# Kernel tuning notes

Hardware: AMD Instinct MI355X
Metric: run time of the kernel (lower is better)

Reference implementation:

```python
import jax, jax.numpy as jnp
import numpy as np

N = 20        # number_of_nodes
K = 2         # Chebyshev order
E_DIM = 4     # embedding_dimensions
OUT = 2       # out_channels
F_IN = 8      # node_features
B = 131072    # batch


def setup_inputs() -> dict:
    key = jax.random.key(0)
    ks = jax.random.split(key, 8)
    x = jax.random.normal(ks[0], (B, N, F_IN), jnp.float32)
    e = jax.random.normal(ks[1], (N, E_DIM), jnp.float32)
    # AVWGCN parameter pools: weights_pool (E_DIM, K, in, out), bias_pool (E_DIM, out)
    gate_w = jax.random.normal(ks[2], (E_DIM, K, F_IN + OUT, 2 * OUT), jnp.float32) * 0.1
    gate_b = jax.random.normal(ks[3], (E_DIM, 2 * OUT), jnp.float32) * 0.1
    upd_w = jax.random.normal(ks[4], (E_DIM, K, F_IN + OUT, OUT), jnp.float32) * 0.1
    upd_b = jax.random.normal(ks[5], (E_DIM, OUT), jnp.float32) * 0.1
    lin_w = jax.random.normal(ks[6], (1, OUT), jnp.float32) * 0.5
    lin_b = jax.random.normal(ks[7], (1,), jnp.float32) * 0.1
    return {"x": x, "e": e, "gate_w": gate_w, "gate_b": gate_b,
            "upd_w": upd_w, "upd_b": upd_b, "lin_w": lin_w, "lin_b": lin_b}


def _avwgcn(x, e, supports, w_pool, b_pool):
    # Node-adaptive weights: (N, K, in, out) and bias (N, out)
    W = jnp.einsum('nd,dkio->nkio', e, w_pool)
    b = e @ b_pool
    # K-hop graph conv gather: (B, N, K, in)
    x_g = jnp.einsum('knm,bmc->bnkc', supports, x)
    return jnp.einsum('bnki,nkio->bno', x_g, W) + b


def reference(x, e, gate_w, gate_b, upd_w, upd_b, lin_w, lin_b):
    dt = x.dtype
    # Adaptive adjacency: softmax(relu(E E^T)) rows; Chebyshev set for K=2 is [I, A]
    A = jax.nn.softmax(jax.nn.relu(e @ e.T), axis=1)
    supports = jnp.stack([jnp.eye(N, dtype=dt), A.astype(dt)])  # (K, N, N)

    H = jnp.zeros((x.shape[0], N, OUT), dt)  # self.h is None -> zeros
    XH = jnp.concatenate([x, H], axis=-1)
    ZR = jax.nn.sigmoid(_avwgcn(XH, e, supports, gate_w, gate_b))
    Z, R = ZR[..., :OUT], ZR[..., OUT:]
    C = jnp.concatenate([x, Z * H], axis=-1)
    HC = jnp.tanh(_avwgcn(C, e, supports, upd_w, upd_b))
    H = R * H + (1.0 - R) * HC

    y = jax.nn.relu(H)
    y = y @ lin_w.T + lin_b
    return y
```

## Files before the change

kernel.cpp:

```cpp
#include <hip/hip_runtime.h>
#include <math.h>

#define NN 20
#define ED 4
#define XROW 160
#define NC 80
#define NKT 5
#define NNT 5
#define FRAG_BYTES (NKT * NNT * 64 * 16)
#define THREADS 512
#define ROWS_PER_WAVE 16
#define ROWS_PER_BLOCK 128
#define TPB 2

typedef __attribute__((ext_vector_type(8))) _Float16 half8;
typedef __attribute__((ext_vector_type(4))) float f32x4;
typedef __attribute__((ext_vector_type(4))) unsigned uint4v;

static __device__ __forceinline__ half8 cvt8(float4 a, float4 b) {
    uint4v u = (uint4v){
        __builtin_bit_cast(unsigned, __builtin_amdgcn_cvt_pkrtz(a.x, a.y)),
        __builtin_bit_cast(unsigned, __builtin_amdgcn_cvt_pkrtz(a.z, a.w)),
        __builtin_bit_cast(unsigned, __builtin_amdgcn_cvt_pkrtz(b.x, b.y)),
        __builtin_bit_cast(unsigned, __builtin_amdgcn_cvt_pkrtz(b.z, b.w))};
    return __builtin_bit_cast(half8, u);
}

static __device__ __forceinline__ float dpp_xor1(float v) {
    return __builtin_bit_cast(float,
        __builtin_amdgcn_mov_dpp(__builtin_bit_cast(int, v), 0xB1, 0xF, 0xF, true));
}
static __device__ __forceinline__ float dpp_xor2(float v) {
    return __builtin_bit_cast(float,
        __builtin_amdgcn_mov_dpp(__builtin_bit_cast(int, v), 0x4E, 0xF, 0xF, true));
}

__global__ __launch_bounds__(THREADS, 4) void rgcn_fused(
        const float* __restrict__ x,
        const float* __restrict__ e,
        const float* __restrict__ gate_w,
        const float* __restrict__ gate_b,
        const float* __restrict__ upd_w,
        const float* __restrict__ upd_b,
        const float* __restrict__ lin_w,
        const float* __restrict__ lin_b,
        float* __restrict__ y) {
    __shared__ __align__(16) char fragmem[FRAG_BYTES];
    __shared__ float sbias[NC];
    __shared__ float el[80];
    __shared__ float sA[400];
    __shared__ float wself[640];
    __shared__ float wagg[640];

    const int t = threadIdx.x;
    const int l = t & 63;
    const int w = t >> 6;

    const size_t rowA = ((size_t)blockIdx.x * TPB + 0) * ROWS_PER_BLOCK + (size_t)w * ROWS_PER_WAVE;
    const size_t rowB = ((size_t)blockIdx.x * TPB + 1) * ROWS_PER_BLOCK + (size_t)w * ROWS_PER_WAVE;
    const float* xpA = x + (rowA + (l & 15)) * XROW + ((l >> 4) << 3);
    const float* xpB = x + (rowB + (l & 15)) * XROW + ((l >> 4) << 3);

    float4 Aa0 = *(const float4*)(xpA);       float4 Ab0 = *(const float4*)(xpA + 4);
    float4 Aa1 = *(const float4*)(xpA + 32);  float4 Ab1 = *(const float4*)(xpA + 36);
    float4 Aa2 = *(const float4*)(xpA + 64);  float4 Ab2 = *(const float4*)(xpA + 68);
    float4 Aa3 = *(const float4*)(xpA + 96);  float4 Ab3 = *(const float4*)(xpA + 100);
    float4 Aa4 = *(const float4*)(xpA + 128); float4 Ab4 = *(const float4*)(xpA + 132);

    if (t < NN * ED) el[t] = e[t];
    __syncthreads();

    if (t < 400) {
        int nn = t / 20, mm = t - (t / 20) * 20;
        float d = 0.f;
        #pragma unroll
        for (int j = 0; j < ED; ++j) d += el[nn * ED + j] * el[mm * ED + j];
        sA[t] = fmaxf(d, 0.f);
    }
    #pragma unroll
    for (int idx = t; idx < 1280; idx += THREADS) {
        int sel = idx >= 640;
        int rem = sel ? idx - 640 : idx;
        int c = rem >> 3, i = rem & 7;
        int n = c >> 2, ro = c & 3;
        float v = 0.f;
        if (ro < 2) {
            int o = 2 + ro;
            #pragma unroll
            for (int d = 0; d < ED; ++d) v += el[n * ED + d] * gate_w[d * 80 + sel * 40 + i * 4 + o];
        } else {
            int o = ro - 2;
            #pragma unroll
            for (int d = 0; d < ED; ++d) v += el[n * ED + d] * upd_w[d * 40 + sel * 20 + i * 2 + o];
        }
        (sel ? wagg : wself)[rem] = v;
    }
    if (t < NC) {
        int n = t >> 2, ro = t & 3;
        float b = 0.f;
        #pragma unroll
        for (int d = 0; d < ED; ++d)
            b += el[n * ED + d] * (ro < 2 ? gate_b[d * 4 + 2 + ro] : upd_b[d * 2 + ro - 2]);
        sbias[t] = b;
    }
    __syncthreads();

    if (t < NN) {
        float mx = -1e30f;
        for (int m = 0; m < NN; ++m) mx = fmaxf(mx, sA[t * 20 + m]);
        float ex[NN]; float sum = 0.f;
        for (int m = 0; m < NN; ++m) { ex[m] = __expf(sA[t * 20 + m] - mx); sum += ex[m]; }
        float inv = 1.f / sum;
        for (int m = 0; m < NN; ++m) sA[t * 20 + m] = ex[m] * inv;
    }
    __syncthreads();

    {
        half8* frag = (half8*)fragmem;
        for (int tile = w; tile < NKT * NNT; tile += 8) {
            int kt = tile / 5, nt = tile - kt * 5;
            int cc = nt * 16 + (l & 15);
            int nn = cc >> 2;
            int mm = kt * 4 + (l >> 4);
            float anm = sA[nn * 20 + mm];
            float4 wg0 = *(const float4*)&wagg[cc * 8];
            float4 wg1 = *(const float4*)&wagg[cc * 8 + 4];
            float v0 = anm * wg0.x, v1 = anm * wg0.y, v2 = anm * wg0.z, v3 = anm * wg0.w;
            float v4 = anm * wg1.x, v5 = anm * wg1.y, v6 = anm * wg1.z, v7 = anm * wg1.w;
            if (nn == mm) {
                float4 ws0 = *(const float4*)&wself[cc * 8];
                float4 ws1 = *(const float4*)&wself[cc * 8 + 4];
                v0 += ws0.x; v1 += ws0.y; v2 += ws0.z; v3 += ws0.w;
                v4 += ws1.x; v5 += ws1.y; v6 += ws1.z; v7 += ws1.w;
            }
            half8 hv;
            hv[0] = (_Float16)v0; hv[1] = (_Float16)v1; hv[2] = (_Float16)v2; hv[3] = (_Float16)v3;
            hv[4] = (_Float16)v4; hv[5] = (_Float16)v5; hv[6] = (_Float16)v6; hv[7] = (_Float16)v7;
            frag[tile * 64 + l] = hv;
        }
    }
    __syncthreads();

    const half8* frag = (const half8*)fragmem;
    const float lw0 = lin_w[0], lw1 = lin_w[1], lb = lin_b[0];
    const int ro = l & 3;
    const bool isR = ro < 2;
    const float myw = (ro & 1) ? lw1 : lw0;

    float4 Ba0 = *(const float4*)(xpB);       float4 Bb0 = *(const float4*)(xpB + 4);
    float4 Ba1 = *(const float4*)(xpB + 32);  float4 Bb1 = *(const float4*)(xpB + 36);
    float4 Ba2 = *(const float4*)(xpB + 64);  float4 Bb2 = *(const float4*)(xpB + 68);
    float4 Ba3 = *(const float4*)(xpB + 96);  float4 Bb3 = *(const float4*)(xpB + 100);
    float4 Ba4 = *(const float4*)(xpB + 128); float4 Bb4 = *(const float4*)(xpB + 132);

    #define STEP(XA, XB, KT, ACC)                                                   \
    {                                                                               \
        half8 a = cvt8(XA, XB);                                                     \
        _Pragma("unroll")                                                           \
        for (int nt = 0; nt < NNT; ++nt) {                                          \
            half8 bh = frag[((KT) * NNT + nt) * 64 + l];                            \
            ACC[nt] = __builtin_amdgcn_mfma_f32_16x16x32_f16(a, bh, ACC[nt], 0, 0, 0); \
        }                                                                           \
    }

    #define EPILOGUE(ACC, ROW0)                                                     \
    {                                                                               \
        const size_t rowb = (ROW0) + ((l >> 4) << 2) + ro;                          \
        _Pragma("unroll")                                                           \
        for (int nt = 0; nt < NNT; ++nt) {                                          \
            const int n = nt * 4 + ((l & 15) >> 2);                                 \
            float ysel = 0.f;                                                       \
            _Pragma("unroll")                                                       \
            for (int q = 0; q < 4; ++q) {                                           \
                float pre = ACC[nt][q];                                             \
                float term;                                                         \
                if (isR) term = __builtin_amdgcn_rcpf(1.f + __expf(pre));           \
                else     term = 1.f - 2.f * __builtin_amdgcn_rcpf(__expf(2.f * pre) + 1.f); \
                float other = dpp_xor2(term);                                       \
                float h = term * other;                                             \
                float s = fmaxf(h, 0.f) * myw;                                      \
                float yq = s + dpp_xor1(s) + lb;                                    \
                if (q == ro) ysel = yq;                                             \
            }                                                                       \
            y[rowb * NN + n] = ysel;                                                \
        }                                                                           \
    }

    {
        f32x4 accA[NNT];
        #pragma unroll
        for (int nt = 0; nt < NNT; ++nt) {
            float b = sbias[nt * 16 + (l & 15)];
            accA[nt] = (f32x4){b, b, b, b};
        }
        STEP(Aa0, Ab0, 0, accA)
        STEP(Aa1, Ab1, 1, accA)
        STEP(Aa2, Ab2, 2, accA)
        STEP(Aa3, Ab3, 3, accA)
        STEP(Aa4, Ab4, 4, accA)
        EPILOGUE(accA, rowA)
    }

    {
        f32x4 accB[NNT];
        #pragma unroll
        for (int nt = 0; nt < NNT; ++nt) {
            float b = sbias[nt * 16 + (l & 15)];
            accB[nt] = (f32x4){b, b, b, b};
        }
        STEP(Ba0, Bb0, 0, accB)
        STEP(Ba1, Bb1, 1, accB)
        STEP(Ba2, Bb2, 2, accB)
        STEP(Ba3, Bb3, 3, accB)
        STEP(Ba4, Bb4, 4, accB)
        EPILOGUE(accB, rowB)
    }
    #undef STEP
    #undef EPILOGUE
}

extern "C" void kernel_launch(void* const* d_in, const int* in_sizes, int n_in,
                              void* d_out, int out_size, void* d_ws, size_t ws_size,
                              hipStream_t stream) {
    const float* x      = (const float*)d_in[0];
    const float* e      = (const float*)d_in[1];
    const float* gate_w = (const float*)d_in[2];
    const float* gate_b = (const float*)d_in[3];
    const float* upd_w  = (const float*)d_in[4];
    const float* upd_b  = (const float*)d_in[5];
    const float* lin_w  = (const float*)d_in[6];
    const float* lin_b  = (const float*)d_in[7];
    float* y = (float*)d_out;

    const int Bn = in_sizes[0] / XROW;
    const int nblocks = Bn / (ROWS_PER_BLOCK * TPB);

    rgcn_fused<<<nblocks, THREADS, 0, stream>>>(x, e, gate_w, gate_b,
                                                upd_w, upd_b, lin_w, lin_b, y);
}
```

Baseline: 24.71 us.

## Process four row chunks per block with software-pipelined x prefetch

Each block now handles four 128-row chunks instead of two, prefetching the next chunk's x registers while computing the current one, and launch bounds are relaxed to 2 blocks per SM. This spreads the per-block setup (adjacency softmax, weight fragment build) over more rows and keeps loads in flight during MFMA and epilogue work. The row softmax is also parallelized across waves with shuffle reductions instead of 20 serial threads. The trade-off is half as many blocks (fewer waves to hide latency) and higher register pressure from double-buffered bursts.

```diff
diff --git a/kernel.cpp b/kernel.cpp
--- a/kernel.cpp
+++ b/kernel.cpp
@@ -10,8 +10,9 @@
 #define FRAG_BYTES (NKT * NNT * 64 * 16)
 #define THREADS 512
 #define ROWS_PER_WAVE 16
-#define ROWS_PER_BLOCK 128
-#define TPB 2
+#define CHUNK_ROWS 128
+#define TPB 4
+#define ROWS_PER_BLOCK (CHUNK_ROWS * TPB)
 
 typedef __attribute__((ext_vector_type(8))) _Float16 half8;
 typedef __attribute__((ext_vector_type(4))) float f32x4;
@@ -35,7 +36,21 @@
         __builtin_amdgcn_mov_dpp(__builtin_bit_cast(int, v), 0x4E, 0xF, 0xF, true));
 }
 
-__global__ __launch_bounds__(THREADS, 4) void rgcn_fused(
+struct Burst {
+    float4 a0, b0, a1, b1, a2, b2, a3, b3, a4, b4;
+};
+
+static __device__ __forceinline__ Burst load_burst(const float* __restrict__ p) {
+    Burst r;
+    r.a0 = *(const float4*)(p);       r.b0 = *(const float4*)(p + 4);
+    r.a1 = *(const float4*)(p + 32);  r.b1 = *(const float4*)(p + 36);
+    r.a2 = *(const float4*)(p + 64);  r.b2 = *(const float4*)(p + 68);
+    r.a3 = *(const float4*)(p + 96);  r.b3 = *(const float4*)(p + 100);
+    r.a4 = *(const float4*)(p + 128); r.b4 = *(const float4*)(p + 132);
+    return r;
+}
+
+__global__ __launch_bounds__(THREADS, 2) void rgcn_fused(
         const float* __restrict__ x,
         const float* __restrict__ e,
         const float* __restrict__ gate_w,
@@ -56,16 +71,11 @@
     const int l = t & 63;
     const int w = t >> 6;
 
-    const size_t rowA = ((size_t)blockIdx.x * TPB + 0) * ROWS_PER_BLOCK + (size_t)w * ROWS_PER_WAVE;
-    const size_t rowB = ((size_t)blockIdx.x * TPB + 1) * ROWS_PER_BLOCK + (size_t)w * ROWS_PER_WAVE;
-    const float* xpA = x + (rowA + (l & 15)) * XROW + ((l >> 4) << 3);
-    const float* xpB = x + (rowB + (l & 15)) * XROW + ((l >> 4) << 3);
-
-    float4 Aa0 = *(const float4*)(xpA);       float4 Ab0 = *(const float4*)(xpA + 4);
-    float4 Aa1 = *(const float4*)(xpA + 32);  float4 Ab1 = *(const float4*)(xpA + 36);
-    float4 Aa2 = *(const float4*)(xpA + 64);  float4 Ab2 = *(const float4*)(xpA + 68);
-    float4 Aa3 = *(const float4*)(xpA + 96);  float4 Ab3 = *(const float4*)(xpA + 100);
-    float4 Aa4 = *(const float4*)(xpA + 128); float4 Ab4 = *(const float4*)(xpA + 132);
+    const size_t base = (size_t)blockIdx.x * ROWS_PER_BLOCK + (size_t)w * ROWS_PER_WAVE;
+    const float* xp = x + (base + (l & 15)) * XROW + ((l >> 4) << 3);
+    const size_t xstep = (size_t)CHUNK_ROWS * XROW;
+
+    Burst cur = load_burst(xp);
 
     if (t < NN * ED) el[t] = e[t];
     __syncthreads();
@@ -105,13 +115,22 @@
     }
     __syncthreads();
 
-    if (t < NN) {
-        float mx = -1e30f;
-        for (int m = 0; m < NN; ++m) mx = fmaxf(mx, sA[t * 20 + m]);
-        float ex[NN]; float sum = 0.f;
-        for (int m = 0; m < NN; ++m) { ex[m] = __expf(sA[t * 20 + m] - mx); sum += ex[m]; }
-        float inv = 1.f / sum;
-        for (int m = 0; m < NN; ++m) sA[t * 20 + m] = ex[m] * inv;
+    {
+        #pragma unroll
+        for (int rep = 0; rep < 3; ++rep) {
+            int r = w + rep * 8;
+            if (r < NN) {
+                float v = (l < NN) ? sA[r * 20 + l] : -1e30f;
+                float mx = v;
+                #pragma unroll
+                for (int s = 32; s >= 1; s >>= 1) mx = fmaxf(mx, __shfl_xor(mx, s));
+                float ex = (l < NN) ? __expf(v - mx) : 0.f;
+                float sum = ex;
+                #pragma unroll
+                for (int s = 32; s >= 1; s >>= 1) sum += __shfl_xor(sum, s);
+                if (l < NN) sA[r * 20 + l] = ex / sum;
+            }
+        }
     }
     __syncthreads();
 
@@ -147,12 +166,6 @@
     const bool isR = ro < 2;
     const float myw = (ro & 1) ? lw1 : lw0;
 
-    float4 Ba0 = *(const float4*)(xpB);       float4 Bb0 = *(const float4*)(xpB + 4);
-    float4 Ba1 = *(const float4*)(xpB + 32);  float4 Bb1 = *(const float4*)(xpB + 36);
-    float4 Ba2 = *(const float4*)(xpB + 64);  float4 Bb2 = *(const float4*)(xpB + 68);
-    float4 Ba3 = *(const float4*)(xpB + 96);  float4 Bb3 = *(const float4*)(xpB + 100);
-    float4 Ba4 = *(const float4*)(xpB + 128); float4 Bb4 = *(const float4*)(xpB + 132);
-
     #define STEP(XA, XB, KT, ACC)                                                   \
     {                                                                               \
         half8 a = cvt8(XA, XB);                                                     \
@@ -163,8 +176,19 @@
         }                                                                           \
     }
 
-    #define EPILOGUE(ACC, ROW0)                                                     \
+    #define COMPUTE(U, ROW0)                                                        \
     {                                                                               \
+        f32x4 acc[NNT];                                                             \
+        _Pragma("unroll")                                                           \
+        for (int nt = 0; nt < NNT; ++nt) {                                          \
+            float b = sbias[nt * 16 + (l & 15)];                                    \
+            acc[nt] = (f32x4){b, b, b, b};                                          \
+        }                                                                           \
+        STEP(U.a0, U.b0, 0, acc)                                                    \
+        STEP(U.a1, U.b1, 1, acc)                                                    \
+        STEP(U.a2, U.b2, 2, acc)                                                    \
+        STEP(U.a3, U.b3, 3, acc)                                                    \
+        STEP(U.a4, U.b4, 4, acc)                                                    \
         const size_t rowb = (ROW0) + ((l >> 4) << 2) + ro;                          \
         _Pragma("unroll")                                                           \
         for (int nt = 0; nt < NNT; ++nt) {                                          \
@@ -172,7 +196,7 @@
             float ysel = 0.f;                                                       \
             _Pragma("unroll")                                                       \
             for (int q = 0; q < 4; ++q) {                                           \
-                float pre = ACC[nt][q];                                             \
+                float pre = acc[nt][q];                                             \
                 float term;                                                         \
                 if (isR) term = __builtin_amdgcn_rcpf(1.f + __expf(pre));           \
                 else     term = 1.f - 2.f * __builtin_amdgcn_rcpf(__expf(2.f * pre) + 1.f); \
@@ -186,37 +210,18 @@
         }                                                                           \
     }
 
-    {
-        f32x4 accA[NNT];
-        #pragma unroll
-        for (int nt = 0; nt < NNT; ++nt) {
-            float b = sbias[nt * 16 + (l & 15)];
-            accA[nt] = (f32x4){b, b, b, b};
-        }
-        STEP(Aa0, Ab0, 0, accA)
-        STEP(Aa1, Ab1, 1, accA)
-        STEP(Aa2, Ab2, 2, accA)
-        STEP(Aa3, Ab3, 3, accA)
-        STEP(Aa4, Ab4, 4, accA)
-        EPILOGUE(accA, rowA)
-    }
-
-    {
-        f32x4 accB[NNT];
-        #pragma unroll
-        for (int nt = 0; nt < NNT; ++nt) {
-            float b = sbias[nt * 16 + (l & 15)];
-            accB[nt] = (f32x4){b, b, b, b};
-        }
-        STEP(Ba0, Bb0, 0, accB)
-        STEP(Ba1, Bb1, 1, accB)
-        STEP(Ba2, Bb2, 2, accB)
-        STEP(Ba3, Bb3, 3, accB)
-        STEP(Ba4, Bb4, 4, accB)
-        EPILOGUE(accB, rowB)
-    }
+    Burst nxt = load_burst(xp + xstep);
+    COMPUTE(cur, base)
+    cur = nxt;
+    nxt = load_burst(xp + 2 * xstep);
+    COMPUTE(cur, base + CHUNK_ROWS)
+    cur = nxt;
+    nxt = load_burst(xp + 3 * xstep);
+    COMPUTE(cur, base + 2 * CHUNK_ROWS)
+    COMPUTE(nxt, base + 3 * CHUNK_ROWS)
+
     #undef STEP
-    #undef EPILOGUE
+    #undef COMPUTE
 }
 
 extern "C" void kernel_launch(void* const* d_in, const int* in_sizes, int n_in,
@@ -233,7 +238,7 @@
     float* y = (float*)d_out;
 
     const int Bn = in_sizes[0] / XROW;
-    const int nblocks = Bn / (ROWS_PER_BLOCK * TPB);
+    const int nblocks = Bn / ROWS_PER_BLOCK;
 
     rgcn_fused<<<nblocks, THREADS, 0, stream>>>(x, e, gate_w, gate_b,
                                                 upd_w, upd_b, lin_w, lin_b, y);
```

Result: slower. 26.83 us (+8.6%).
